# Kernel optimization log

Measured on AMD Instinct MI355X. Metric: run time of the kernel, lower is better.

Reference implementation:

```python
import jax, jax.numpy as jnp
import numpy as np
from jax import lax

B, L, H = 2, 4096, 2048
NH = 16
DK = H // NH  # num_slot = 128 (q/k dim)
C = 64        # chunk size
EPS = 1e-5
N_LAYER = 24


def setup_inputs() -> dict:
    key = jax.random.key(0)
    ks = jax.random.split(key, 7)
    std = 0.02
    return {
        "hidden_states": jax.random.normal(ks[0], (B, L, H), jnp.float32),
        "Wq": jax.random.normal(ks[1], (DK, H), jnp.float32) * std,
        "Wk": jax.random.normal(ks[2], (DK, H), jnp.float32) * std,
        "Wog": jax.random.normal(ks[3], (H, H), jnp.float32) * std,
        "Wig": jax.random.normal(ks[4], (H, H), jnp.float32) * std,
        "Wo": jax.random.normal(ks[5], (H, H), jnp.float32) * (std / np.sqrt(2 * N_LAYER)),
        "g_norm_w": jnp.ones((H,), jnp.float32),
    }


def _gla_chunk(q, k, v, gf):
    # q,k,gf: [b,L,dk]; v: [b,L,dv]. Recurrence: S_t = diag(exp(gf_t)) S_{t-1} + k_t v_t^T; o_t = q_t S_t
    b, Ls, dk = q.shape
    dv = v.shape[-1]
    n = Ls // C
    # [n, b, C, d] so scan iterates over chunks
    qc = q.reshape(b, n, C, dk).transpose(1, 0, 2, 3)
    kc = k.reshape(b, n, C, dk).transpose(1, 0, 2, 3)
    vc = v.reshape(b, n, C, dv).transpose(1, 0, 2, 3)
    gc = gf.reshape(b, n, C, dk).transpose(1, 0, 2, 3)
    Bc = jnp.cumsum(gc, axis=2)  # inclusive within-chunk log-decay

    tril = jnp.tril(jnp.ones((C, C), bool))

    def step(S, inp):
        qh, kh, vh, Bh = inp  # [b,C,dk],[b,C,dk],[b,C,dv],[b,C,dk]
        Blast = Bh[:, -1, :]  # [b,dk]
        # exp(B_i - B_j) <= 1 for j <= i (gf < 0): numerically safe pairwise form
        D = Bh[:, :, None, :] - Bh[:, None, :, :]  # [b,C,C,dk]
        A = jnp.einsum('bid,bjd,bijd->bij', qh, kh, jnp.exp(D))
        A = jnp.where(tril, A, 0.0)
        o_intra = jnp.einsum('bij,bjv->biv', A, vh)
        o_inter = jnp.einsum('bid,bdv->biv', qh * jnp.exp(Bh), S)
        kd = kh * jnp.exp(Blast[:, None, :] - Bh)  # <= 1 scaling, safe
        S_new = S * jnp.exp(Blast)[..., None] + jnp.einsum('bjd,bjv->bdv', kd, vh)
        return S_new, o_intra + o_inter

    S0 = jnp.zeros((b, dk, dv), q.dtype)
    _, o = lax.scan(step, S0, (qc, kc, vc, Bc))  # o: [n,b,C,dv]
    return o.transpose(1, 0, 2, 3).reshape(b, Ls, dv)


def reference(hidden_states, Wq, Wk, Wog, Wig, Wo, g_norm_w):
    x = hidden_states
    q = jax.nn.softmax(x @ Wq.T, axis=-1)        # [b,L,dk]
    k = jax.nn.sigmoid(x @ Wk.T)                 # [b,L,dk]
    v = x                                        # value_dim == hidden_size
    gf = jax.nn.log_sigmoid(-k)                  # per-key-dim log decay, in (-1.32, -0.69)
    o = _gla_chunk(q, k, v, gf)                  # [b,L,H]
    # output gate: og_proj(o) + ig_proj(x), fused RMSNorm + swish gate
    go = o @ Wog.T + x @ Wig.T
    on = o * lax.rsqrt(jnp.mean(o * o, axis=-1, keepdims=True) + EPS) * g_norm_w
    o = on * (go * jax.nn.sigmoid(go))
    return o @ Wo.T
```

## Files before the change

### kernel.cpp

```cpp
#include <hip/hip_runtime.h>
#include <hip/hip_bf16.h>

typedef __hip_bfloat16 bf16;
typedef __bf16 bf16x8 __attribute__((ext_vector_type(8)));
typedef float f32x4 __attribute__((ext_vector_type(4)));

__device__ __forceinline__ void async16(void* lds_base, const void* g) {
  __builtin_amdgcn_global_load_lds(
      (const __attribute__((address_space(1))) void*)g,
      (__attribute__((address_space(3))) void*)lds_base, 16, 0, 0);
}

__global__ void cvt_bf16_kernel(const float* __restrict__ s, bf16* __restrict__ d, int n4) {
  const int i = blockIdx.x * 256 + threadIdx.x;
  if (i >= n4) return;
  const float4 v = ((const float4*)s)[i];
  bf16 h0 = __float2bfloat16(v.x), h1 = __float2bfloat16(v.y);
  bf16 h2 = __float2bfloat16(v.z), h3 = __float2bfloat16(v.w);
  ushort4 o;
  o.x = *(unsigned short*)&h0; o.y = *(unsigned short*)&h1;
  o.z = *(unsigned short*)&h2; o.w = *(unsigned short*)&h3;
  *(ushort4*)((unsigned short*)d + (size_t)i * 4) = o;
}

__global__ __launch_bounds__(256) void convert_x_kernel(
    const float* __restrict__ x, bf16* __restrict__ xb, bf16* __restrict__ xbT) {
  __shared__ float tile[64][65];
  const int b = blockIdx.z;
  const int l0 = blockIdx.x * 64, d0 = blockIdx.y * 64;
  const int t = threadIdx.x;
  const int c = t & 63, r4 = t >> 6;
  const size_t base = ((size_t)b * 4096 + l0) * 2048 + d0;
#pragma unroll
  for (int i = 0; i < 16; ++i) {
    const int row = i * 4 + r4;
    const float v = x[base + (size_t)row * 2048 + c];
    tile[row][c] = v;
    xb[base + (size_t)row * 2048 + c] = __float2bfloat16(v);
  }
  __syncthreads();
  const size_t baseT = ((size_t)b * 2048 + d0) * 4096 + l0;
#pragma unroll
  for (int i = 0; i < 16; ++i) {
    const int dr = i * 4 + r4;
    xbT[baseT + (size_t)dr * 4096 + c] = __float2bfloat16(tile[c][dr]);
  }
}

template <int MODE>
__global__ __launch_bounds__(256, 2) void gemm_bt(
    const bf16* __restrict__ A0, const bf16* __restrict__ B0,
    const bf16* __restrict__ A1, const bf16* __restrict__ B1,
    float* __restrict__ outf, bf16* __restrict__ outb,
    const bf16* __restrict__ o_in, const float* __restrict__ rmsv,
    const float* __restrict__ gnw, int M, int N, int K) {
  __shared__ bf16 lA[128 * 32];
  __shared__ bf16 lB[128 * 32];
  const int tid = threadIdx.x;
  const int lane = tid & 63, wave = tid >> 6;
  const int l15 = lane & 15, l4 = lane >> 4;
  const int bm = blockIdx.x * 128, bn = blockIdx.y * 128;
  const int wm = (wave & 1) * 64, wn = (wave >> 1) * 64;
  const int srow = tid >> 2;
  const int skc = (tid & 3) * 8;

  const f32x4 fz = {0.f, 0.f, 0.f, 0.f};
  f32x4 acc[4][4];
#pragma unroll
  for (int i = 0; i < 4; ++i)
#pragma unroll
    for (int j = 0; j < 4; ++j) acc[i][j] = fz;

  bf16* lAu  = lA + wave * 512;
  bf16* lAu2 = lA + 2048 + wave * 512;
  bf16* lBu  = lB + wave * 512;
  bf16* lBu2 = lB + 2048 + wave * 512;

  const int npass = (MODE == 1) ? 2 : 1;
  for (int pass = 0; pass < npass; ++pass) {
    const bf16* Ap = (pass == 0) ? A0 : A1;
    const bf16* Bp = (pass == 0) ? B0 : B1;
    const bf16* gA0 = Ap + (size_t)(bm + srow) * K + skc;
    const bf16* gA1 = Ap + (size_t)(bm + srow + 64) * K + skc;
    const bf16* gB0 = Bp + (size_t)(bn + srow) * K + skc;
    const bf16* gB1 = Bp + (size_t)(bn + srow + 64) * K + skc;
    for (int k0 = 0; k0 < K; k0 += 32) {
      __syncthreads();
      async16(lAu, gA0 + k0);
      async16(lAu2, gA1 + k0);
      async16(lBu, gB0 + k0);
      async16(lBu2, gB1 + k0);
      __syncthreads();
      bf16x8 af[4], bfv[4];
#pragma unroll
      for (int mt = 0; mt < 4; ++mt)
        af[mt] = *(const bf16x8*)(lA + (wm + mt * 16 + l15) * 32 + l4 * 8);
#pragma unroll
      for (int nt = 0; nt < 4; ++nt)
        bfv[nt] = *(const bf16x8*)(lB + (wn + nt * 16 + l15) * 32 + l4 * 8);
#pragma unroll
      for (int mt = 0; mt < 4; ++mt)
#pragma unroll
        for (int nt = 0; nt < 4; ++nt)
          acc[mt][nt] = __builtin_amdgcn_mfma_f32_16x16x32_bf16(af[mt], bfv[nt], acc[mt][nt], 0, 0, 0);
    }
  }

#pragma unroll
  for (int mt = 0; mt < 4; ++mt)
#pragma unroll
    for (int r = 0; r < 4; ++r) {
      const int gr = bm + wm + mt * 16 + l4 * 4 + r;
#pragma unroll
      for (int nt = 0; nt < 4; ++nt) {
        const int gc = bn + wn + nt * 16 + l15;
        const float v = acc[mt][nt][r];
        if (MODE == 1) {
          const float o = (float)o_in[(size_t)gr * N + gc];
          const float on = o * rmsv[gr] * gnw[gc];
          const float sw = v / (1.f + __expf(-v));
          outb[(size_t)gr * N + gc] = __float2bfloat16(on * sw);
        } else {
          outf[(size_t)gr * N + gc] = v;
        }
      }
    }
}

#define QMFMA(AF, BF, MH, NH)                                               \
  do {                                                                      \
    __builtin_amdgcn_s_setprio(1);                                          \
    _Pragma("unroll") for (int ks_ = 0; ks_ < 2; ++ks_) {                   \
      _Pragma("unroll") for (int mt_ = 0; mt_ < 4; ++mt_) {                 \
        _Pragma("unroll") for (int nt_ = 0; nt_ < 2; ++nt_)                 \
            acc[(MH) * 4 + mt_][(NH) * 2 + nt_] =                           \
                __builtin_amdgcn_mfma_f32_16x16x32_bf16(                    \
                    AF[mt_][ks_], BF[nt_][ks_],                             \
                    acc[(MH) * 4 + mt_][(NH) * 2 + nt_], 0, 0, 0);          \
      }                                                                     \
    }                                                                       \
    __builtin_amdgcn_s_setprio(0);                                          \
  } while (0)

template <int MODE>
__global__ __launch_bounds__(512, 2) void gemm256(
    const bf16* __restrict__ A0, const bf16* __restrict__ B0,
    const bf16* __restrict__ A1, const bf16* __restrict__ B1,
    float* __restrict__ outf, bf16* __restrict__ outb,
    const bf16* __restrict__ o_in, const float* __restrict__ rmsv,
    const float* __restrict__ gnw, int M, int N) {
  __shared__ bf16 lA[2][16384];
  __shared__ bf16 lB[2][16384];
  const int tid = threadIdx.x;
  const int lane = tid & 63;
  const int wave = tid >> 6;
  const int wmi = wave >> 2;
  const int wni = wave & 3;
  const int l15 = lane & 15, l4 = lane >> 4;
  const int axor = l15 & 7;

  const int nwg = gridDim.x;
  const int cpx = nwg >> 3;
  int wg = blockIdx.x;
  wg = (wg & 7) * cpx + (wg >> 3);
  const int NBN = N >> 8;
  const int bm = (wg / NBN) * 256;
  const int bn = (wg % NBN) * 256;

  const int srow = tid >> 3;
  const int scol = ((tid & 7) ^ (srow & 7)) * 8;
  const size_t goff = (size_t)srow * 2048 + scol;

  const int NT = (MODE == 1) ? 64 : 32;

  const bf16* Abase0 = A0 + (size_t)bm * 2048;
  const bf16* Abase1 = (MODE == 1) ? (A1 + (size_t)bm * 2048) : A0;
  const bf16* Bbase0 = B0 + (size_t)bn * 2048;
  const bf16* Bbase1 = (MODE == 1) ? (B1 + (size_t)bn * 2048) : B0;

  auto stageA = [&](int kt, int h, int buf) {
    int t = (kt < NT) ? kt : (NT - 1);
    const bf16* src = Abase0;
    int k0 = t * 64;
    if (MODE == 1 && t >= 32) { src = Abase1; k0 = (t - 32) * 64; }
    const bf16* g = src + (size_t)h * 128 * 2048 + k0 + goff;
    bf16* d = &lA[buf][h * 8192] + tid * 8;
    async16(d, g);
    async16(d + 4096, g + (size_t)64 * 2048);
  };
  auto stageB = [&](int kt, int h, int buf) {
    int t = (kt < NT) ? kt : (NT - 1);
    const bf16* src = Bbase0;
    int k0 = t * 64;
    if (MODE == 1 && t >= 32) { src = Bbase1; k0 = (t - 32) * 64; }
    const bf16* g = src + (size_t)h * 128 * 2048 + k0 + goff;
    bf16* d = &lB[buf][h * 8192] + tid * 8;
    async16(d, g);
    async16(d + 4096, g + (size_t)64 * 2048);
  };

  auto readA = [&](bf16x8 (&af)[4][2], int buf, int mh) {
    const bf16* base = &lA[buf][wmi * 8192];
#pragma unroll
    for (int mt = 0; mt < 4; ++mt)
#pragma unroll
      for (int ks = 0; ks < 2; ++ks)
        af[mt][ks] = *(const bf16x8*)(base + (mh * 64 + mt * 16 + l15) * 64 +
                                      (((ks * 4 + l4) ^ axor) << 3));
  };
  auto readB = [&](bf16x8 (&bb)[2][2], int buf, int nh) {
    const bf16* base = &lB[buf][(wni >> 1) * 8192];
#pragma unroll
    for (int nt = 0; nt < 2; ++nt)
#pragma unroll
      for (int ks = 0; ks < 2; ++ks)
        bb[nt][ks] = *(const bf16x8*)(base +
                                      ((wni & 1) * 64 + nh * 32 + nt * 16 + l15) * 64 +
                                      (((ks * 4 + l4) ^ axor) << 3));
  };

  const f32x4 fz = {0.f, 0.f, 0.f, 0.f};
  f32x4 acc[8][4];
#pragma unroll
  for (int i = 0; i < 8; ++i)
#pragma unroll
    for (int j = 0; j < 4; ++j) acc[i][j] = fz;

  stageB(0, 0, 0); stageB(0, 1, 0);
  stageA(0, 0, 0); stageA(0, 1, 0);
  stageB(1, 0, 1); stageB(1, 1, 1);
  asm volatile("s_waitcnt vmcnt(4)" ::: "memory");
  __builtin_amdgcn_s_barrier();

  bf16x8 aF[4][2], b0F[2][2], b1F[2][2];

  for (int kt = 0; kt < NT; ++kt) {
    const int cur = kt & 1, nxt = cur ^ 1;
    readA(aF, cur, 0);
    readB(b0F, cur, 0);
    stageA(kt + 1, 0, nxt);
    __builtin_amdgcn_s_barrier();
    asm volatile("s_waitcnt lgkmcnt(0)" ::: "memory");
    QMFMA(aF, b0F, 0, 0);
    __builtin_amdgcn_s_barrier();
    readB(b1F, cur, 1);
    stageA(kt + 1, 1, nxt);
    __builtin_amdgcn_s_barrier();
    asm volatile("s_waitcnt lgkmcnt(0)" ::: "memory");
    QMFMA(aF, b1F, 0, 1);
    __builtin_amdgcn_s_barrier();
    readA(aF, cur, 1);
    stageB(kt + 2, 0, cur);
    __builtin_amdgcn_s_barrier();
    asm volatile("s_waitcnt lgkmcnt(0)" ::: "memory");
    QMFMA(aF, b0F, 1, 0);
    __builtin_amdgcn_s_barrier();
    stageB(kt + 2, 1, cur);
    asm volatile("s_waitcnt vmcnt(4)" ::: "memory");
    __builtin_amdgcn_s_barrier();
    QMFMA(aF, b1F, 1, 1);
    __builtin_amdgcn_s_barrier();
    __builtin_amdgcn_sched_barrier(0);
  }

#pragma unroll
  for (int i = 0; i < 8; ++i) {
#pragma unroll
    for (int r = 0; r < 4; ++r) {
      const int gr = bm + wmi * 128 + i * 16 + l4 * 4 + r;
#pragma unroll
      for (int j = 0; j < 4; ++j) {
        const int gc = bn + wni * 64 + j * 16 + l15;
        const float v = acc[i][j][r];
        if (MODE == 1) {
          const float o = (float)o_in[(size_t)gr * N + gc];
          const float on = o * rmsv[gr] * gnw[gc];
          const float sw = v / (1.f + __expf(-v));
          outb[(size_t)gr * N + gc] = __float2bfloat16(on * sw);
        } else {
          outf[(size_t)gr * N + gc] = v;
        }
      }
    }
  }
}

__global__ __launch_bounds__(64) void qk_post_kernel(
    const float* __restrict__ logits, bf16* __restrict__ qb,
    bf16* __restrict__ kb, float* __restrict__ gfl) {
  const int row = blockIdx.x;
  const int t = threadIdx.x;
  const float* lr = logits + (size_t)row * 256;
  float a0 = lr[t], a1 = lr[t + 64];
  float m = fmaxf(a0, a1);
#pragma unroll
  for (int s = 32; s; s >>= 1) m = fmaxf(m, __shfl_xor(m, s));
  float e0 = __expf(a0 - m), e1 = __expf(a1 - m);
  float sum = e0 + e1;
#pragma unroll
  for (int s = 32; s; s >>= 1) sum += __shfl_xor(sum, s);
  const float inv = 1.f / sum;
  qb[(size_t)row * 128 + t]      = __float2bfloat16(e0 * inv);
  qb[(size_t)row * 128 + t + 64] = __float2bfloat16(e1 * inv);
  float b0 = lr[128 + t], b1 = lr[128 + t + 64];
  float k0 = 1.f / (1.f + __expf(-b0));
  float k1 = 1.f / (1.f + __expf(-b1));
  kb[(size_t)row * 128 + t]      = __float2bfloat16(k0);
  kb[(size_t)row * 128 + t + 64] = __float2bfloat16(k1);
  gfl[(size_t)row * 128 + t]      = -log1pf(__expf(k0));
  gfl[(size_t)row * 128 + t + 64] = -log1pf(__expf(k1));
}

__global__ __launch_bounds__(256, 2) void gla_kernel(
    const bf16* __restrict__ qb, const bf16* __restrict__ kb,
    const float* __restrict__ gfl, const bf16* __restrict__ xbT,
    bf16* __restrict__ ob, float* __restrict__ rmsv) {
  __shared__ bf16 sF1[64][136];
  __shared__ bf16 sF2[128][136];
  __shared__ float sM[128];
  __shared__ float rowsq[64];
  const int tid = threadIdx.x;
  const int lane = tid & 63, wave = tid >> 6;
  const int l15 = lane & 15, l4 = lane >> 4;
  const int chunk = blockIdx.x, b = blockIdx.y;
  const int row0 = b * 4096 + chunk * 64;

  if (tid < 64) rowsq[tid] = 0.f;

  if (tid < 128) {
    float s = 0.f;
    for (int i = 0; i <= 32; ++i) s += gfl[(size_t)(row0 + i) * 128 + tid];
    sM[tid] = s;
  }
  __syncthreads();

  if (tid < 128) {
    const int d = tid;
    const float M = sM[d];
    float bi = 0.f;
    for (int i = 0; i < 64; ++i) {
      bi += gfl[(size_t)(row0 + i) * 128 + d];
      const float q = (float)qb[(size_t)(row0 + i) * 128 + d];
      const float k = (float)kb[(size_t)(row0 + i) * 128 + d];
      sF1[i][d]      = __float2bfloat16(q * __expf(bi - M));
      sF2[64 + i][d] = __float2bfloat16(k * __expf(M - bi));
    }
  } else {
    const int d = tid - 128;
    if (chunk == 0) {
      for (int j = 0; j < 64; ++j) sF2[j][d] = __float2bfloat16(0.f);
    } else {
      const float M = sM[d];
      float bw = 0.f;
      for (int j = 63; j >= 0; --j) {
        const float k = (float)kb[(size_t)(row0 - 64 + j) * 128 + d];
        sF2[j][d] = __float2bfloat16(k * __expf(M - bw));
        bw -= gfl[(size_t)(row0 - 64 + j) * 128 + d];
      }
    }
  }
  __syncthreads();

  const f32x4 fz = {0.f, 0.f, 0.f, 0.f};
  {
    f32x4 sacc[4][2];
#pragma unroll
    for (int mt = 0; mt < 4; ++mt) { sacc[mt][0] = fz; sacc[mt][1] = fz; }
    bf16x8 f1[4][4];
#pragma unroll
    for (int kt = 0; kt < 4; ++kt)
#pragma unroll
      for (int mt = 0; mt < 4; ++mt)
        f1[kt][mt] = *(const bf16x8*)(&sF1[mt * 16 + l15][kt * 32 + l4 * 8]);
#pragma unroll
    for (int nt = 0; nt < 2; ++nt)
#pragma unroll
      for (int kt = 0; kt < 4; ++kt) {
        const bf16x8 f2 = *(const bf16x8*)(&sF2[wave * 32 + nt * 16 + l15][kt * 32 + l4 * 8]);
#pragma unroll
        for (int mt = 0; mt < 4; ++mt)
          sacc[mt][nt] = __builtin_amdgcn_mfma_f32_16x16x32_bf16(f1[kt][mt], f2, sacc[mt][nt], 0, 0, 0);
      }
    __syncthreads();
#pragma unroll
    for (int mt = 0; mt < 4; ++mt)
#pragma unroll
      for (int nt = 0; nt < 2; ++nt)
#pragma unroll
        for (int r = 0; r < 4; ++r) {
          const int i = mt * 16 + l4 * 4 + r;
          const int jw = wave * 32 + nt * 16 + l15;
          const bool ok = (jw < 64) || (jw - 64 <= i);
          sF1[i][jw] = __float2bfloat16(ok ? sacc[mt][nt][r] : 0.f);
        }
    __syncthreads();
  }

  bf16x8 av[4][4];
#pragma unroll
  for (int kt = 0; kt < 4; ++kt)
#pragma unroll
    for (int mt = 0; mt < 4; ++mt)
      av[kt][mt] = *(const bf16x8*)(&sF1[mt * 16 + l15][kt * 32 + l4 * 8]);

  float rs[4][4];
#pragma unroll
  for (int a = 0; a < 4; ++a)
#pragma unroll
    for (int r2 = 0; r2 < 4; ++r2) rs[a][r2] = 0.f;

  const int lwb = chunk * 64 - 64;
  for (int dt = 0; dt < 8; ++dt) {
    const int c0 = dt * 256 + wave * 64;
    f32x4 oacc[4][4];
#pragma unroll
    for (int mt = 0; mt < 4; ++mt)
#pragma unroll
      for (int nt = 0; nt < 4; ++nt) oacc[mt][nt] = fz;
#pragma unroll
    for (int kt = 0; kt < 4; ++kt)
#pragma unroll
      for (int nt = 0; nt < 4; ++nt) {
        const int dv = c0 + nt * 16 + l15;
        int lw = lwb + kt * 32 + l4 * 8;
        if (lw < 0) lw = 0;
        const bf16x8 vv = *(const bf16x8*)(xbT + ((size_t)b * 2048 + dv) * 4096 + lw);
#pragma unroll
        for (int mt = 0; mt < 4; ++mt)
          oacc[mt][nt] = __builtin_amdgcn_mfma_f32_16x16x32_bf16(av[kt][mt], vv, oacc[mt][nt], 0, 0, 0);
      }
#pragma unroll
    for (int mt = 0; mt < 4; ++mt)
#pragma unroll
      for (int r = 0; r < 4; ++r) {
        const int i = mt * 16 + l4 * 4 + r;
#pragma unroll
        for (int nt = 0; nt < 4; ++nt) {
          const float v = oacc[mt][nt][r];
          ob[(size_t)(row0 + i) * 2048 + (c0 + nt * 16 + l15)] = __float2bfloat16(v);
          rs[mt][r] += v * v;
        }
      }
  }

#pragma unroll
  for (int mt = 0; mt < 4; ++mt)
#pragma unroll
    for (int r = 0; r < 4; ++r) {
      float v = rs[mt][r];
      v += __shfl_xor(v, 1); v += __shfl_xor(v, 2);
      v += __shfl_xor(v, 4); v += __shfl_xor(v, 8);
      if (l15 == 0) atomicAdd(&rowsq[mt * 16 + l4 * 4 + r], v);
    }
  __syncthreads();
  if (tid < 64)
    rmsv[row0 + tid] = rsqrtf(rowsq[tid] * (1.f / 2048.f) + 1e-5f);
}

extern "C" void kernel_launch(void* const* d_in, const int* in_sizes, int n_in,
                              void* d_out, int out_size, void* d_ws, size_t ws_size,
                              hipStream_t stream) {
  const float* x   = (const float*)d_in[0];
  const float* Wq  = (const float*)d_in[1];
  const float* Wk  = (const float*)d_in[2];
  const float* Wog = (const float*)d_in[3];
  const float* Wig = (const float*)d_in[4];
  const float* Wo  = (const float*)d_in[5];
  const float* gnw = (const float*)d_in[6];
  float* out = (float*)d_out;

  char* w = (char*)d_ws;
  auto alloc = [&](size_t bytes) {
    char* p = w;
    w += (bytes + 255) & ~(size_t)255;
    return p;
  };
  bf16*  wqkb   = (bf16*)alloc((size_t)256 * 2048 * 2);
  bf16*  wogb   = (bf16*)alloc((size_t)2048 * 2048 * 2);
  bf16*  wigb   = (bf16*)alloc((size_t)2048 * 2048 * 2);
  bf16*  wob    = (bf16*)alloc((size_t)2048 * 2048 * 2);
  bf16*  xb     = (bf16*)alloc((size_t)8192 * 2048 * 2);
  bf16*  xbT    = (bf16*)alloc((size_t)8192 * 2048 * 2);
  float* logits = (float*)alloc((size_t)8192 * 256 * 4);
  bf16*  qbuf   = (bf16*)alloc((size_t)8192 * 128 * 2);
  bf16*  kbuf   = (bf16*)alloc((size_t)8192 * 128 * 2);
  float* gfbuf  = (float*)alloc((size_t)8192 * 128 * 4);
  bf16*  obuf   = (bf16*)alloc((size_t)8192 * 2048 * 2);
  float* rmsbuf = (float*)alloc((size_t)8192 * 4);
  bf16*  gatedb = xbT;

  cvt_bf16_kernel<<<dim3((65536 + 255) / 256), 256, 0, stream>>>(Wq, wqkb, 65536);
  cvt_bf16_kernel<<<dim3((65536 + 255) / 256), 256, 0, stream>>>(Wk, wqkb + 262144, 65536);
  cvt_bf16_kernel<<<dim3((1048576 + 255) / 256), 256, 0, stream>>>(Wog, wogb, 1048576);
  cvt_bf16_kernel<<<dim3((1048576 + 255) / 256), 256, 0, stream>>>(Wig, wigb, 1048576);
  cvt_bf16_kernel<<<dim3((1048576 + 255) / 256), 256, 0, stream>>>(Wo, wob, 1048576);

  convert_x_kernel<<<dim3(64, 32, 2), 256, 0, stream>>>(x, xb, xbT);

  gemm_bt<0><<<dim3(64, 2), 256, 0, stream>>>(
      xb, wqkb, nullptr, nullptr, logits, nullptr, nullptr, nullptr, nullptr,
      8192, 256, 2048);

  qk_post_kernel<<<dim3(8192), 64, 0, stream>>>(logits, qbuf, kbuf, gfbuf);

  gla_kernel<<<dim3(64, 2), 256, 0, stream>>>(qbuf, kbuf, gfbuf, xbT, obuf, rmsbuf);

  gemm256<1><<<dim3(256), 512, 0, stream>>>(
      obuf, wogb, xb, wigb, nullptr, gatedb, obuf, rmsbuf, gnw, 8192, 2048);

  gemm256<2><<<dim3(256), 512, 0, stream>>>(
      gatedb, wob, nullptr, nullptr, out, nullptr, nullptr, nullptr, nullptr,
      8192, 2048);

  (void)in_sizes; (void)n_in; (void)out_size; (void)ws_size;
}
```

Measured before the change: 469.0 us.

## Concatenate o/x and Wog/Wig along K, split GLA output columns over two blocks

Stores the GLA output and bf16 x side by side in one [8192,4096] buffer, with the matching Wog/Wig weights concatenated into [2048,4096]. The gate GEMM then becomes a single K=4096 GEMM with no per-stage source switching. The GLA kernel grid gains a z dimension that splits the 2048 value columns across two blocks for more parallelism; RMS sums are accumulated atomically and the rsqrt moves into the GEMM epilogue. Also vectorizes the x conversion/transpose kernel and unrolls the gemm256 K loop by two with extra scheduling barriers and waitcnts, at the cost of duplicated chunk-state work in GLA.

```diff
diff --git a/kernel.cpp b/kernel.cpp
--- a/kernel.cpp
+++ b/kernel.cpp
@@ -23,37 +23,59 @@
   *(ushort4*)((unsigned short*)d + (size_t)i * 4) = o;
 }
 
+__global__ void cvt_bf16_strided(const float* __restrict__ s, bf16* __restrict__ d, int n4) {
+  const int i = blockIdx.x * 256 + threadIdx.x;
+  if (i >= n4) return;
+  const int row = i >> 9;
+  const int col4 = i & 511;
+  const float4 v = ((const float4*)s)[i];
+  bf16 h0 = __float2bfloat16(v.x), h1 = __float2bfloat16(v.y);
+  bf16 h2 = __float2bfloat16(v.z), h3 = __float2bfloat16(v.w);
+  ushort4 o;
+  o.x = *(unsigned short*)&h0; o.y = *(unsigned short*)&h1;
+  o.z = *(unsigned short*)&h2; o.w = *(unsigned short*)&h3;
+  *(ushort4*)((unsigned short*)d + (size_t)row * 4096 + col4 * 4) = o;
+}
+
 __global__ __launch_bounds__(256) void convert_x_kernel(
-    const float* __restrict__ x, bf16* __restrict__ xb, bf16* __restrict__ xbT) {
+    const float* __restrict__ x, bf16* __restrict__ comb, bf16* __restrict__ xbT) {
   __shared__ float tile[64][65];
   const int b = blockIdx.z;
   const int l0 = blockIdx.x * 64, d0 = blockIdx.y * 64;
   const int t = threadIdx.x;
-  const int c = t & 63, r4 = t >> 6;
+  const int c4 = (t & 15) * 4, r = t >> 4;
   const size_t base = ((size_t)b * 4096 + l0) * 2048 + d0;
 #pragma unroll
-  for (int i = 0; i < 16; ++i) {
-    const int row = i * 4 + r4;
-    const float v = x[base + (size_t)row * 2048 + c];
-    tile[row][c] = v;
-    xb[base + (size_t)row * 2048 + c] = __float2bfloat16(v);
+  for (int i = 0; i < 4; ++i) {
+    const int row = i * 16 + r;
+    const float4 v = *(const float4*)(x + base + (size_t)row * 2048 + c4);
+    tile[row][c4 + 0] = v.x; tile[row][c4 + 1] = v.y;
+    tile[row][c4 + 2] = v.z; tile[row][c4 + 3] = v.w;
+    bf16 h0 = __float2bfloat16(v.x), h1 = __float2bfloat16(v.y);
+    bf16 h2 = __float2bfloat16(v.z), h3 = __float2bfloat16(v.w);
+    ushort4 o;
+    o.x = *(unsigned short*)&h0; o.y = *(unsigned short*)&h1;
+    o.z = *(unsigned short*)&h2; o.w = *(unsigned short*)&h3;
+    *(ushort4*)(comb + ((size_t)(b * 4096 + l0 + row)) * 4096 + 2048 + d0 + c4) = o;
   }
   __syncthreads();
-  const size_t baseT = ((size_t)b * 2048 + d0) * 4096 + l0;
-#pragma unroll
-  for (int i = 0; i < 16; ++i) {
-    const int dr = i * 4 + r4;
-    xbT[baseT + (size_t)dr * 4096 + c] = __float2bfloat16(tile[c][dr]);
-  }
-}
-
-template <int MODE>
-__global__ __launch_bounds__(256, 2) void gemm_bt(
-    const bf16* __restrict__ A0, const bf16* __restrict__ B0,
-    const bf16* __restrict__ A1, const bf16* __restrict__ B1,
-    float* __restrict__ outf, bf16* __restrict__ outb,
-    const bf16* __restrict__ o_in, const float* __restrict__ rmsv,
-    const float* __restrict__ gnw, int M, int N, int K) {
+#pragma unroll
+  for (int i = 0; i < 4; ++i) {
+    const int d = i * 16 + r;
+    bf16 h0 = __float2bfloat16(tile[c4 + 0][d]);
+    bf16 h1 = __float2bfloat16(tile[c4 + 1][d]);
+    bf16 h2 = __float2bfloat16(tile[c4 + 2][d]);
+    bf16 h3 = __float2bfloat16(tile[c4 + 3][d]);
+    ushort4 o;
+    o.x = *(unsigned short*)&h0; o.y = *(unsigned short*)&h1;
+    o.z = *(unsigned short*)&h2; o.w = *(unsigned short*)&h3;
+    *(ushort4*)(xbT + ((size_t)(b * 2048 + d0 + d)) * 4096 + l0 + c4) = o;
+  }
+}
+
+__global__ __launch_bounds__(256, 2) void gemm_logits(
+    const bf16* __restrict__ A, const bf16* __restrict__ B,
+    float* __restrict__ outf, int lda, int N, int K) {
   __shared__ bf16 lA[128 * 32];
   __shared__ bf16 lB[128 * 32];
   const int tid = threadIdx.x;
@@ -76,34 +98,29 @@
   bf16* lBu  = lB + wave * 512;
   bf16* lBu2 = lB + 2048 + wave * 512;
 
-  const int npass = (MODE == 1) ? 2 : 1;
-  for (int pass = 0; pass < npass; ++pass) {
-    const bf16* Ap = (pass == 0) ? A0 : A1;
-    const bf16* Bp = (pass == 0) ? B0 : B1;
-    const bf16* gA0 = Ap + (size_t)(bm + srow) * K + skc;
-    const bf16* gA1 = Ap + (size_t)(bm + srow + 64) * K + skc;
-    const bf16* gB0 = Bp + (size_t)(bn + srow) * K + skc;
-    const bf16* gB1 = Bp + (size_t)(bn + srow + 64) * K + skc;
-    for (int k0 = 0; k0 < K; k0 += 32) {
-      __syncthreads();
-      async16(lAu, gA0 + k0);
-      async16(lAu2, gA1 + k0);
-      async16(lBu, gB0 + k0);
-      async16(lBu2, gB1 + k0);
-      __syncthreads();
-      bf16x8 af[4], bfv[4];
-#pragma unroll
-      for (int mt = 0; mt < 4; ++mt)
-        af[mt] = *(const bf16x8*)(lA + (wm + mt * 16 + l15) * 32 + l4 * 8);
+  const bf16* gA0 = A + (size_t)(bm + srow) * lda + skc;
+  const bf16* gA1 = A + (size_t)(bm + srow + 64) * lda + skc;
+  const bf16* gB0 = B + (size_t)(bn + srow) * K + skc;
+  const bf16* gB1 = B + (size_t)(bn + srow + 64) * K + skc;
+  for (int k0 = 0; k0 < K; k0 += 32) {
+    __syncthreads();
+    async16(lAu, gA0 + k0);
+    async16(lAu2, gA1 + k0);
+    async16(lBu, gB0 + k0);
+    async16(lBu2, gB1 + k0);
+    __syncthreads();
+    bf16x8 af[4], bfv[4];
+#pragma unroll
+    for (int mt = 0; mt < 4; ++mt)
+      af[mt] = *(const bf16x8*)(lA + (wm + mt * 16 + l15) * 32 + l4 * 8);
+#pragma unroll
+    for (int nt = 0; nt < 4; ++nt)
+      bfv[nt] = *(const bf16x8*)(lB + (wn + nt * 16 + l15) * 32 + l4 * 8);
+#pragma unroll
+    for (int mt = 0; mt < 4; ++mt)
 #pragma unroll
       for (int nt = 0; nt < 4; ++nt)
-        bfv[nt] = *(const bf16x8*)(lB + (wn + nt * 16 + l15) * 32 + l4 * 8);
-#pragma unroll
-      for (int mt = 0; mt < 4; ++mt)
-#pragma unroll
-        for (int nt = 0; nt < 4; ++nt)
-          acc[mt][nt] = __builtin_amdgcn_mfma_f32_16x16x32_bf16(af[mt], bfv[nt], acc[mt][nt], 0, 0, 0);
-    }
+        acc[mt][nt] = __builtin_amdgcn_mfma_f32_16x16x32_bf16(af[mt], bfv[nt], acc[mt][nt], 0, 0, 0);
   }
 
 #pragma unroll
@@ -114,15 +131,7 @@
 #pragma unroll
       for (int nt = 0; nt < 4; ++nt) {
         const int gc = bn + wn + nt * 16 + l15;
-        const float v = acc[mt][nt][r];
-        if (MODE == 1) {
-          const float o = (float)o_in[(size_t)gr * N + gc];
-          const float on = o * rmsv[gr] * gnw[gc];
-          const float sw = v / (1.f + __expf(-v));
-          outb[(size_t)gr * N + gc] = __float2bfloat16(on * sw);
-        } else {
-          outf[(size_t)gr * N + gc] = v;
-        }
+        outf[(size_t)gr * N + gc] = acc[mt][nt][r];
       }
     }
 }
@@ -144,11 +153,10 @@
 
 template <int MODE>
 __global__ __launch_bounds__(512, 2) void gemm256(
-    const bf16* __restrict__ A0, const bf16* __restrict__ B0,
-    const bf16* __restrict__ A1, const bf16* __restrict__ B1,
+    const bf16* __restrict__ A, const bf16* __restrict__ B,
     float* __restrict__ outf, bf16* __restrict__ outb,
-    const bf16* __restrict__ o_in, const float* __restrict__ rmsv,
-    const float* __restrict__ gnw, int M, int N) {
+    const bf16* __restrict__ o_in, const float* __restrict__ rmssum,
+    const float* __restrict__ gnw, int N, int K, int ostr) {
   __shared__ bf16 lA[2][16384];
   __shared__ bf16 lB[2][16384];
   const int tid = threadIdx.x;
@@ -169,34 +177,25 @@
 
   const int srow = tid >> 3;
   const int scol = ((tid & 7) ^ (srow & 7)) * 8;
-  const size_t goff = (size_t)srow * 2048 + scol;
-
-  const int NT = (MODE == 1) ? 64 : 32;
-
-  const bf16* Abase0 = A0 + (size_t)bm * 2048;
-  const bf16* Abase1 = (MODE == 1) ? (A1 + (size_t)bm * 2048) : A0;
-  const bf16* Bbase0 = B0 + (size_t)bn * 2048;
-  const bf16* Bbase1 = (MODE == 1) ? (B1 + (size_t)bn * 2048) : B0;
+  const size_t goff = (size_t)srow * K + scol;
+  const int NT = K >> 6;
+
+  const bf16* Ab = A + (size_t)bm * K + goff;
+  const bf16* Bb = B + (size_t)bn * K + goff;
 
   auto stageA = [&](int kt, int h, int buf) {
-    int t = (kt < NT) ? kt : (NT - 1);
-    const bf16* src = Abase0;
-    int k0 = t * 64;
-    if (MODE == 1 && t >= 32) { src = Abase1; k0 = (t - 32) * 64; }
-    const bf16* g = src + (size_t)h * 128 * 2048 + k0 + goff;
+    const int t = (kt < NT) ? kt : (NT - 1);
+    const bf16* g = Ab + (size_t)h * 128 * K + t * 64;
     bf16* d = &lA[buf][h * 8192] + tid * 8;
     async16(d, g);
-    async16(d + 4096, g + (size_t)64 * 2048);
+    async16(d + 4096, g + (size_t)64 * K);
   };
   auto stageB = [&](int kt, int h, int buf) {
-    int t = (kt < NT) ? kt : (NT - 1);
-    const bf16* src = Bbase0;
-    int k0 = t * 64;
-    if (MODE == 1 && t >= 32) { src = Bbase1; k0 = (t - 32) * 64; }
-    const bf16* g = src + (size_t)h * 128 * 2048 + k0 + goff;
+    const int t = (kt < NT) ? kt : (NT - 1);
+    const bf16* g = Bb + (size_t)h * 128 * K + t * 64;
     bf16* d = &lB[buf][h * 8192] + tid * 8;
     async16(d, g);
-    async16(d + 4096, g + (size_t)64 * 2048);
+    async16(d + 4096, g + (size_t)64 * K);
   };
 
   auto readA = [&](bf16x8 (&af)[4][2], int buf, int mh) {
@@ -231,14 +230,15 @@
   stageB(1, 0, 1); stageB(1, 1, 1);
   asm volatile("s_waitcnt vmcnt(4)" ::: "memory");
   __builtin_amdgcn_s_barrier();
+  __builtin_amdgcn_sched_barrier(0);
 
   bf16x8 aF[4][2], b0F[2][2], b1F[2][2];
 
-  for (int kt = 0; kt < NT; ++kt) {
-    const int cur = kt & 1, nxt = cur ^ 1;
+  auto ktile = [&](int kt, int cur, int nxt) {
     readA(aF, cur, 0);
     readB(b0F, cur, 0);
     stageA(kt + 1, 0, nxt);
+    asm volatile("s_waitcnt lgkmcnt(8)" ::: "memory");
     __builtin_amdgcn_s_barrier();
     asm volatile("s_waitcnt lgkmcnt(0)" ::: "memory");
     QMFMA(aF, b0F, 0, 0);
@@ -258,9 +258,14 @@
     stageB(kt + 2, 1, cur);
     asm volatile("s_waitcnt vmcnt(4)" ::: "memory");
     __builtin_amdgcn_s_barrier();
+    __builtin_amdgcn_sched_barrier(0);
     QMFMA(aF, b1F, 1, 1);
     __builtin_amdgcn_s_barrier();
-    __builtin_amdgcn_sched_barrier(0);
+  };
+
+  for (int kt = 0; kt < NT; kt += 2) {
+    ktile(kt, 0, 1);
+    ktile(kt + 1, 1, 0);
   }
 
 #pragma unroll
@@ -268,13 +273,15 @@
 #pragma unroll
     for (int r = 0; r < 4; ++r) {
       const int gr = bm + wmi * 128 + i * 16 + l4 * 4 + r;
+      float rinv = 0.f;
+      if (MODE == 1) rinv = rsqrtf(rmssum[gr] * (1.f / 2048.f) + 1e-5f);
 #pragma unroll
       for (int j = 0; j < 4; ++j) {
         const int gc = bn + wni * 64 + j * 16 + l15;
         const float v = acc[i][j][r];
         if (MODE == 1) {
-          const float o = (float)o_in[(size_t)gr * N + gc];
-          const float on = o * rmsv[gr] * gnw[gc];
+          const float o = (float)o_in[(size_t)gr * ostr + gc];
+          const float on = o * rinv * gnw[gc];
           const float sw = v / (1.f + __expf(-v));
           outb[(size_t)gr * N + gc] = __float2bfloat16(on * sw);
         } else {
@@ -287,9 +294,10 @@
 
 __global__ __launch_bounds__(64) void qk_post_kernel(
     const float* __restrict__ logits, bf16* __restrict__ qb,
-    bf16* __restrict__ kb, float* __restrict__ gfl) {
+    bf16* __restrict__ kb, float* __restrict__ gfl, float* __restrict__ rmssum) {
   const int row = blockIdx.x;
   const int t = threadIdx.x;
+  if (t == 0) rmssum[row] = 0.f;
   const float* lr = logits + (size_t)row * 256;
   float a0 = lr[t], a1 = lr[t + 64];
   float m = fmaxf(a0, a1);
@@ -314,7 +322,7 @@
 __global__ __launch_bounds__(256, 2) void gla_kernel(
     const bf16* __restrict__ qb, const bf16* __restrict__ kb,
     const float* __restrict__ gfl, const bf16* __restrict__ xbT,
-    bf16* __restrict__ ob, float* __restrict__ rmsv) {
+    bf16* __restrict__ ob, float* __restrict__ rmssum) {
   __shared__ bf16 sF1[64][136];
   __shared__ bf16 sF2[128][136];
   __shared__ float sM[128];
@@ -322,7 +330,7 @@
   const int tid = threadIdx.x;
   const int lane = tid & 63, wave = tid >> 6;
   const int l15 = lane & 15, l4 = lane >> 4;
-  const int chunk = blockIdx.x, b = blockIdx.y;
+  const int chunk = blockIdx.x, b = blockIdx.y, z = blockIdx.z;
   const int row0 = b * 4096 + chunk * 64;
 
   if (tid < 64) rowsq[tid] = 0.f;
@@ -410,7 +418,7 @@
     for (int r2 = 0; r2 < 4; ++r2) rs[a][r2] = 0.f;
 
   const int lwb = chunk * 64 - 64;
-  for (int dt = 0; dt < 8; ++dt) {
+  for (int dt = z * 4; dt < z * 4 + 4; ++dt) {
     const int c0 = dt * 256 + wave * 64;
     f32x4 oacc[4][4];
 #pragma unroll
@@ -437,7 +445,7 @@
 #pragma unroll
         for (int nt = 0; nt < 4; ++nt) {
           const float v = oacc[mt][nt][r];
-          ob[(size_t)(row0 + i) * 2048 + (c0 + nt * 16 + l15)] = __float2bfloat16(v);
+          ob[(size_t)(row0 + i) * 4096 + (c0 + nt * 16 + l15)] = __float2bfloat16(v);
           rs[mt][r] += v * v;
         }
       }
@@ -454,7 +462,7 @@
     }
   __syncthreads();
   if (tid < 64)
-    rmsv[row0 + tid] = rsqrtf(rowsq[tid] * (1.f / 2048.f) + 1e-5f);
+    atomicAdd(&rmssum[row0 + tid], rowsq[tid]);
 }
 
 extern "C" void kernel_launch(void* const* d_in, const int* in_sizes, int n_in,
@@ -476,41 +484,37 @@
     return p;
   };
   bf16*  wqkb   = (bf16*)alloc((size_t)256 * 2048 * 2);
-  bf16*  wogb   = (bf16*)alloc((size_t)2048 * 2048 * 2);
-  bf16*  wigb   = (bf16*)alloc((size_t)2048 * 2048 * 2);
+  bf16*  wcomb  = (bf16*)alloc((size_t)2048 * 4096 * 2);
   bf16*  wob    = (bf16*)alloc((size_t)2048 * 2048 * 2);
-  bf16*  xb     = (bf16*)alloc((size_t)8192 * 2048 * 2);
+  bf16*  acomb  = (bf16*)alloc((size_t)8192 * 4096 * 2);
   bf16*  xbT    = (bf16*)alloc((size_t)8192 * 2048 * 2);
   float* logits = (float*)alloc((size_t)8192 * 256 * 4);
   bf16*  qbuf   = (bf16*)alloc((size_t)8192 * 128 * 2);
   bf16*  kbuf   = (bf16*)alloc((size_t)8192 * 128 * 2);
   float* gfbuf  = (float*)alloc((size_t)8192 * 128 * 4);
-  bf16*  obuf   = (bf16*)alloc((size_t)8192 * 2048 * 2);
   float* rmsbuf = (float*)alloc((size_t)8192 * 4);
   bf16*  gatedb = xbT;
 
   cvt_bf16_kernel<<<dim3((65536 + 255) / 256), 256, 0, stream>>>(Wq, wqkb, 65536);
   cvt_bf16_kernel<<<dim3((65536 + 255) / 256), 256, 0, stream>>>(Wk, wqkb + 262144, 65536);
-  cvt_bf16_kernel<<<dim3((1048576 + 255) / 256), 256, 0, stream>>>(Wog, wogb, 1048576);
-  cvt_bf16_kernel<<<dim3((1048576 + 255) / 256), 256, 0, stream>>>(Wig, wigb, 1048576);
+  cvt_bf16_strided<<<dim3((1048576 + 255) / 256), 256, 0, stream>>>(Wog, wcomb, 1048576);
+  cvt_bf16_strided<<<dim3((1048576 + 255) / 256), 256, 0, stream>>>(Wig, wcomb + 2048, 1048576);
   cvt_bf16_kernel<<<dim3((1048576 + 255) / 256), 256, 0, stream>>>(Wo, wob, 1048576);
 
-  convert_x_kernel<<<dim3(64, 32, 2), 256, 0, stream>>>(x, xb, xbT);
-
-  gemm_bt<0><<<dim3(64, 2), 256, 0, stream>>>(
-      xb, wqkb, nullptr, nullptr, logits, nullptr, nullptr, nullptr, nullptr,
-      8192, 256, 2048);
-
-  qk_post_kernel<<<dim3(8192), 64, 0, stream>>>(logits, qbuf, kbuf, gfbuf);
-
-  gla_kernel<<<dim3(64, 2), 256, 0, stream>>>(qbuf, kbuf, gfbuf, xbT, obuf, rmsbuf);
+  convert_x_kernel<<<dim3(64, 32, 2), 256, 0, stream>>>(x, acomb, xbT);
+
+  gemm_logits<<<dim3(64, 2), 256, 0, stream>>>(
+      acomb + 2048, wqkb, logits, 4096, 256, 2048);
+
+  qk_post_kernel<<<dim3(8192), 64, 0, stream>>>(logits, qbuf, kbuf, gfbuf, rmsbuf);
+
+  gla_kernel<<<dim3(64, 2, 2), 256, 0, stream>>>(qbuf, kbuf, gfbuf, xbT, acomb, rmsbuf);
 
   gemm256<1><<<dim3(256), 512, 0, stream>>>(
-      obuf, wogb, xb, wigb, nullptr, gatedb, obuf, rmsbuf, gnw, 8192, 2048);
+      acomb, wcomb, nullptr, gatedb, acomb, rmsbuf, gnw, 2048, 4096, 4096);
 
   gemm256<2><<<dim3(256), 512, 0, stream>>>(
-      gatedb, wob, nullptr, nullptr, out, nullptr, nullptr, nullptr, nullptr,
-      8192, 2048);
+      gatedb, wob, out, nullptr, nullptr, nullptr, nullptr, 2048, 2048, 2048);
 
   (void)in_sizes; (void)n_in; (void)out_size; (void)ws_size;
 }
```

Result: no change. 473.3 us (+0.9%).
